# Kernel tuning notes

Hardware: AMD Instinct MI355X
Metric: run time of the kernel (lower is better)

## Reference

```python
import jax, jax.numpy as jnp
import numpy as np

BN_EPS = 1e-5


def _mlp_layer(x, W, b, gamma, beta):
    # x: [B, N, Cin]; Conv1d(k=1) == per-point linear, then BatchNorm1d over (B,N), ReLU
    y = jnp.einsum('bnc,oc->bno', x, W) + b  # [B, N, Cout]
    mean = y.mean(axis=(0, 1))
    var = y.var(axis=(0, 1))
    y = (y - mean) * jax.lax.rsqrt(var + BN_EPS) * gamma + beta
    return jax.nn.relu(y)


def setup_inputs() -> dict:
    key = jax.random.key(0)
    ks = jax.random.split(key, 12)
    B, N, M, C1, C2 = 4, 16384, 4096, 64, 256
    Cin = C1 + C2  # 320
    H1, H2 = 256, 128
    inp = {
        'xyz_fine': jax.random.normal(ks[0], (B, N, 3), jnp.float32),
        'xyz_coarse': jax.random.normal(ks[1], (B, M, 3), jnp.float32),
        'feats_fine': jax.random.normal(ks[2], (B, N, C1), jnp.float32),
        'feats_coarse': jax.random.normal(ks[3], (B, M, C2), jnp.float32),
        'W1': jax.random.normal(ks[4], (H1, Cin), jnp.float32) * (1.0 / np.sqrt(Cin)),
        'b1': jnp.zeros((H1,), jnp.float32),
        'g1': jnp.ones((H1,), jnp.float32),
        'be1': jnp.zeros((H1,), jnp.float32),
        'W2': jax.random.normal(ks[5], (H2, H1), jnp.float32) * (1.0 / np.sqrt(H1)),
        'b2': jnp.zeros((H2,), jnp.float32),
        'g2': jnp.ones((H2,), jnp.float32),
        'be2': jnp.zeros((H2,), jnp.float32),
    }
    return inp


def reference(xyz_fine, xyz_coarse, feats_fine, feats_coarse,
              W1, b1, g1, be1, W2, b2, g2, be2):
    # squared pairwise distance: [B, N, M]
    d = (jnp.sum(xyz_fine ** 2, -1, keepdims=True)
         - 2.0 * jnp.einsum('bnd,bmd->bnm', xyz_fine, xyz_coarse)
         + jnp.sum(xyz_coarse ** 2, -1)[:, None, :])
    # 3 smallest distances
    neg_d, idx = jax.lax.top_k(-d, 3)        # idx: [B, N, 3]
    dists = jnp.maximum(-neg_d, 1e-10)
    w = 1.0 / dists
    w = w / jnp.sum(w, -1, keepdims=True)    # [B, N, 3]
    # gather coarse features: [B, N, 3, C2]
    gathered = jax.vmap(lambda f, i: f[i])(feats_coarse, idx)
    interp = jnp.einsum('bnk,bnkc->bnc', w, gathered)  # [B, N, C2]
    x = jnp.concatenate([interp, feats_fine], axis=-1)  # [B, N, Cin]
    x = _mlp_layer(x, W1, b1, g1, be1)
    x = _mlp_layer(x, W2, b2, g2, be2)
    return x  # [B, N, 128]
```

## Files before the change

kernel.cpp:

```cpp
#include <hip/hip_runtime.h>
#include <hip/hip_bf16.h>
#include <stdint.h>

#define B_    4
#define N_    16384
#define M_    4096
#define C1_   64
#define C2_   256
#define CIN_  320
#define H1_   256
#define H2_   128
#define ROWS_ (B_*N_)
#define SPLIT_ 4
#define CHUNK_ (M_/SPLIT_)

typedef __attribute__((ext_vector_type(8))) short bf16x8;
typedef __attribute__((ext_vector_type(4))) float f32x4;
typedef __attribute__((ext_vector_type(8))) unsigned short u16x8;
typedef __attribute__((ext_vector_type(4))) unsigned short u16x4;

static __device__ __forceinline__ unsigned short f2bf(float f) {
  union { float f; unsigned u; } v; v.f = f;
  unsigned r = v.u + 0x7fffu + ((v.u >> 16) & 1u);
  return (unsigned short)(r >> 16);
}
static __device__ __forceinline__ float bf2f(unsigned short h) {
  union { unsigned u; float f; } v; v.u = ((unsigned)h) << 16;
  return v.f;
}

static __device__ __forceinline__ void gload16(const void* g, void* lds) {
  __builtin_amdgcn_global_load_lds(
      (__attribute__((address_space(1))) void*)(uintptr_t)g,
      (__attribute__((address_space(3))) void*)(uintptr_t)lds,
      16, 0, 0);
}

#define INS3(dv, iv) do {                                        \
  float _d = (dv); int _ii = (iv);                               \
  if (_d < d3) {                                                 \
    if (_d < d2) {                                               \
      d3 = d2; i3 = i2;                                          \
      if (_d < d1) { d2 = d1; i2 = i1; d1 = _d; i1 = _ii; }      \
      else         { d2 = _d; i2 = _ii; }                        \
    } else { d3 = _d; i3 = _ii; }                                \
  } } while (0)

__global__ __launch_bounds__(256) void prep(
    const float* __restrict__ W1, const float* __restrict__ W2,
    const float* __restrict__ xyzc, const float* __restrict__ fc,
    unsigned short* __restrict__ W1b, unsigned short* __restrict__ W2b,
    float4* __restrict__ cpk, unsigned short* __restrict__ fcb)
{
  int i = blockIdx.x * 256 + threadIdx.x;
  if (i < H1_*CIN_) W1b[i] = f2bf(W1[i]);
  if (i < H2_*H1_)  W2b[i] = f2bf(W2[i]);
  if (i < B_*M_) {
    float x = xyzc[i*3], y = xyzc[i*3+1], z = xyzc[i*3+2];
    cpk[i] = make_float4(x, y, z, x*x + y*y + z*z);
  }
  const int total4 = B_*M_*C2_/4;
  const int stride = gridDim.x * 256;
  for (int t = i; t < total4; t += stride) {
    float4 v = ((const float4*)fc)[t];
    u16x4 o;
    o[0] = f2bf(v.x); o[1] = f2bf(v.y); o[2] = f2bf(v.z); o[3] = f2bf(v.w);
    ((u16x4*)fcb)[t] = o;
  }
}

__global__ __launch_bounds__(256) void nn_scan(
    const float* __restrict__ xyzf, const float4* __restrict__ cpk,
    float4* __restrict__ pdw, int4* __restrict__ piw)
{
  __shared__ float4 cp[CHUNK_];
  const int tid  = threadIdx.x;
  const int s    = blockIdx.x & (SPLIT_-1);
  const int tile = (blockIdx.x >> 2) & 63;
  const int b    = blockIdx.x >> 8;

  const float4* src = cpk + (size_t)b * M_ + s * CHUNK_;
  for (int i = tid; i < CHUNK_; i += 256) cp[i] = src[i];
  __syncthreads();

  const int p = tile * 256 + tid;
  const size_t gp = (size_t)b * N_ + p;
  const float* xf = xyzf + gp * 3;
  const float fx = xf[0], fy = xf[1], fz = xf[2];
  const float xx = fx*fx + fy*fy + fz*fz;
  const float nx = -2.f*fx, ny = -2.f*fy, nz = -2.f*fz;

  float d1 = 3.4e38f, d2 = 3.4e38f, d3 = 3.4e38f;
  int   i1 = 0, i2 = 0, i3 = 0;

  #pragma unroll 1
  for (int g = 0; g < CHUNK_; g += 8) {
    float dd[8];
    #pragma unroll
    for (int u = 0; u < 8; ++u) {
      float4 c = cp[g + u];
      dd[u] = xx + fmaf(nx, c.x, fmaf(ny, c.y, fmaf(nz, c.z, c.w)));
    }
    #pragma unroll
    for (int u = 0; u < 8; ++u) {
      float d = dd[u]; int j = g + u;
      if (d < d3) {
        bool c1 = d < d1, c2 = d < d2;
        d3 = c2 ? d2 : d;              i3 = c2 ? i2 : j;
        d2 = c1 ? d1 : (c2 ? d : d2);  i2 = c1 ? i1 : (c2 ? j : i2);
        d1 = c1 ? d  : d1;             i1 = c1 ? j  : i1;
      }
    }
  }
  const int base = s * CHUNK_;
  pdw[(size_t)s * ROWS_ + gp] = make_float4(d1, d2, d3, 0.f);
  piw[(size_t)s * ROWS_ + gp] = make_int4(i1 + base, i2 + base, i3 + base, 0);
}

__global__ __launch_bounds__(256) void nn_finish(
    const float4* __restrict__ pdw, const int4* __restrict__ piw,
    const float* __restrict__ ff, const unsigned short* __restrict__ fcb,
    unsigned short* __restrict__ X)
{
  __shared__ float wv[64][3];
  __shared__ int   wi[64][3];
  const int tid  = threadIdx.x;
  const int b    = blockIdx.x >> 8;
  const int tile = blockIdx.x & 255;
  const size_t gp0 = (size_t)b * N_ + tile * 64;

  if (tid < 64) {
    const size_t gp = gp0 + tid;
    float d1 = 3.4e38f, d2 = 3.4e38f, d3 = 3.4e38f;
    int   i1 = 0, i2 = 0, i3 = 0;
    #pragma unroll
    for (int s = 0; s < SPLIT_; ++s) {
      float4 dv = pdw[(size_t)s * ROWS_ + gp];
      int4   iv = piw[(size_t)s * ROWS_ + gp];
      INS3(dv.x, iv.x);
      INS3(dv.y, iv.y);
      INS3(dv.z, iv.z);
    }
    d1 = fmaxf(d1, 1e-10f); d2 = fmaxf(d2, 1e-10f); d3 = fmaxf(d3, 1e-10f);
    float u1 = 1.f/d1, u2 = 1.f/d2, u3 = 1.f/d3;
    float inv = 1.f/(u1 + u2 + u3);
    wv[tid][0] = u1*inv; wv[tid][1] = u2*inv; wv[tid][2] = u3*inv;
    wi[tid][0] = i1;     wi[tid][1] = i2;     wi[tid][2] = i3;
  }
  __syncthreads();

  const int w = tid >> 6, l = tid & 63;
  const unsigned short* fcb_b = fcb + (size_t)b * M_ * C2_;
  unsigned short* Xb = X + gp0 * CIN_;
  #pragma unroll 2
  for (int q = 0; q < 16; ++q) {
    int pl = w * 16 + q;
    float a1 = wv[pl][0], a2 = wv[pl][1], a3 = wv[pl][2];
    int   j1 = wi[pl][0], j2 = wi[pl][1], j3 = wi[pl][2];
    u16x4 r1 = ((const u16x4*)(fcb_b + (size_t)j1 * C2_))[l];
    u16x4 r2 = ((const u16x4*)(fcb_b + (size_t)j2 * C2_))[l];
    u16x4 r3 = ((const u16x4*)(fcb_b + (size_t)j3 * C2_))[l];
    u16x4 o;
    #pragma unroll
    for (int e = 0; e < 4; ++e) {
      float v = fmaf(a1, bf2f(r1[e]), fmaf(a2, bf2f(r2[e]), a3 * bf2f(r3[e])));
      o[e] = f2bf(v);
    }
    *(u16x4*)(Xb + (size_t)pl * CIN_ + l * 4) = o;
  }

  {
    const float* ffb = ff + gp0 * C1_;
    int pl = tid >> 2, c0 = (tid & 3) * 16;
    const float4* fsrc = (const float4*)(ffb + (size_t)pl * C1_ + c0);
    unsigned short* dst = Xb + (size_t)pl * CIN_ + C2_ + c0;
    #pragma unroll
    for (int t = 0; t < 4; ++t) {
      float4 v = fsrc[t];
      u16x4 o;
      o[0] = f2bf(v.x); o[1] = f2bf(v.y); o[2] = f2bf(v.z); o[3] = f2bf(v.w);
      *(u16x4*)(dst + t * 4) = o;
    }
  }
}

template<int K, int NTOT, bool OUTBF>
__global__ __launch_bounds__(256) void gemm_stats(
    const unsigned short* __restrict__ A,
    const unsigned short* __restrict__ Bw,
    unsigned short* __restrict__ Yb,
    float* __restrict__ Yf,
    float* __restrict__ part)
{
  constexpr int BM = 128, BN = 128, BK = 64;
  constexpr int NCT = NTOT / BN;
  __shared__ unsigned short As[BM*BK];
  __shared__ unsigned short Bs[BN*BK];
  __shared__ float sred[2][BN][2];

  const int tid = threadIdx.x;
  const int l   = tid & 63;
  const int w   = tid >> 6;
  const int wm  = w >> 1, wn = w & 1;
  int rt, ct;
  if (NCT == 2) {
    rt = (blockIdx.x & 7) | ((blockIdx.x >> 4) << 3);
    ct = (blockIdx.x >> 3) & 1;
  } else {
    rt = blockIdx.x / NCT; ct = blockIdx.x % NCT;
  }
  const int lr  = l & 15;
  const int lk  = (l >> 4) * 8;

  const unsigned short* Arow = A  + (size_t)rt * BM * K;
  const unsigned short* Brow = Bw + (size_t)ct * BN * K;

  f32x4 acc[4][4] = {};

  for (int k0 = 0; k0 < K; k0 += BK) {
    #pragma unroll
    for (int q = 0; q < 4; ++q) {
      int chunk = q * 256 + tid;
      int row = chunk >> 3, cc = chunk & 7;
      unsigned ldsoff = (unsigned)(q * 256 + (tid & ~63)) * 16u;
      gload16(Arow + (size_t)row * K + k0 + cc * 8, (char*)As + ldsoff);
      gload16(Brow + (size_t)row * K + k0 + cc * 8, (char*)Bs + ldsoff);
    }
    __syncthreads();
    #pragma unroll
    for (int kk = 0; kk < BK/32; ++kk) {
      bf16x8 af[4], bfr[4];
      #pragma unroll
      for (int m = 0; m < 4; ++m)
        af[m] = *(const bf16x8*)(As + (wm*64 + m*16 + lr)*BK + kk*32 + lk);
      #pragma unroll
      for (int n = 0; n < 4; ++n)
        bfr[n] = *(const bf16x8*)(Bs + (wn*64 + n*16 + lr)*BK + kk*32 + lk);
      #pragma unroll
      for (int m = 0; m < 4; ++m)
        #pragma unroll
        for (int n = 0; n < 4; ++n)
          acc[m][n] = __builtin_amdgcn_mfma_f32_16x16x32_bf16(af[m], bfr[n], acc[m][n], 0, 0, 0);
    }
    __syncthreads();
  }

  const int orow0 = rt*BM + wm*64;
  const int ocol0 = ct*BN + wn*64;
  #pragma unroll
  for (int n = 0; n < 4; ++n) {
    float s = 0.f, qq = 0.f;
    #pragma unroll
    for (int m = 0; m < 4; ++m) {
      #pragma unroll
      for (int r = 0; r < 4; ++r) {
        float v = acc[m][n][r];
        int row = orow0 + m*16 + (l >> 4)*4 + r;
        int col = ocol0 + n*16 + lr;
        size_t off = (size_t)row * NTOT + col;
        if (OUTBF) Yb[off] = f2bf(v); else Yf[off] = v;
        s += v; qq += v*v;
      }
    }
    s  += __shfl_xor(s, 16);  s  += __shfl_xor(s, 32);
    qq += __shfl_xor(qq, 16); qq += __shfl_xor(qq, 32);
    if (l < 16) {
      sred[wm][wn*64 + n*16 + l][0] = s;
      sred[wm][wn*64 + n*16 + l][1] = qq;
    }
  }
  __syncthreads();
  if (tid < BN) {
    float S = sred[0][tid][0] + sred[1][tid][0];
    float Q = sred[0][tid][1] + sred[1][tid][1];
    part[((size_t)rt * NTOT + ct*BN + tid) * 2 + 0] = S;
    part[((size_t)rt * NTOT + ct*BN + tid) * 2 + 1] = Q;
  }
}

template<int K, int NTOT>
__global__ __launch_bounds__(256) void gemm_bnrelu_stats(
    const unsigned short* __restrict__ Yin,
    const float* __restrict__ ab,
    const unsigned short* __restrict__ Bw,
    unsigned short* __restrict__ Yb,
    float* __restrict__ part)
{
  constexpr int BM = 128, BN = 128, BK = 64;
  constexpr int NCT = NTOT / BN;
  __shared__ unsigned short As[BM*BK];
  __shared__ unsigned short Bs[BN*BK];
  __shared__ float sa[K], sb[K];
  __shared__ float sred[2][BN][2];

  const int tid = threadIdx.x;
  const int l   = tid & 63;
  const int w   = tid >> 6;
  const int wm  = w >> 1, wn = w & 1;
  const int rt  = blockIdx.x / NCT, ct = blockIdx.x % NCT;
  const int lr  = l & 15;
  const int lk  = (l >> 4) * 8;
  const int cc  = tid & 7;
  const int r0  = tid >> 3;

  sa[tid] = ab[tid*2];
  sb[tid] = ab[tid*2 + 1];

  const unsigned short* Arow = Yin + (size_t)rt * BM * K;
  const unsigned short* Brow = Bw  + (size_t)ct * BN * K;

  f32x4 acc[4][4] = {};
  __syncthreads();

  for (int k0 = 0; k0 < K; k0 += BK) {
    #pragma unroll
    for (int q = 0; q < 4; ++q) {
      int chunk = q * 256 + tid;
      int row = chunk >> 3, c8 = chunk & 7;
      unsigned ldsoff = (unsigned)(q * 256 + (tid & ~63)) * 16u;
      gload16(Brow + (size_t)row * K + k0 + c8 * 8, (char*)Bs + ldsoff);
    }
    float a_[8], b_[8];
    *(float4*)&a_[0] = *(const float4*)&sa[k0 + cc*8];
    *(float4*)&a_[4] = *(const float4*)&sa[k0 + cc*8 + 4];
    *(float4*)&b_[0] = *(const float4*)&sb[k0 + cc*8];
    *(float4*)&b_[4] = *(const float4*)&sb[k0 + cc*8 + 4];
    #pragma unroll
    for (int q = 0; q < 4; ++q) {
      int row = q*32 + r0;
      u16x8 v = *(const u16x8*)(Arow + (size_t)row * K + k0 + cc*8);
      u16x8 o;
      #pragma unroll
      for (int e = 0; e < 8; ++e) {
        float f = fmaxf(fmaf(bf2f((unsigned short)v[e]), a_[e], b_[e]), 0.f);
        o[e] = f2bf(f);
      }
      *(u16x8*)((char*)As + (unsigned)(q*256 + tid) * 16u) = o;
    }
    __syncthreads();
    #pragma unroll
    for (int kk = 0; kk < BK/32; ++kk) {
      bf16x8 af[4], bfr[4];
      #pragma unroll
      for (int m = 0; m < 4; ++m)
        af[m] = *(const bf16x8*)(As + (wm*64 + m*16 + lr)*BK + kk*32 + lk);
      #pragma unroll
      for (int n = 0; n < 4; ++n)
        bfr[n] = *(const bf16x8*)(Bs + (wn*64 + n*16 + lr)*BK + kk*32 + lk);
      #pragma unroll
      for (int m = 0; m < 4; ++m)
        #pragma unroll
        for (int n = 0; n < 4; ++n)
          acc[m][n] = __builtin_amdgcn_mfma_f32_16x16x32_bf16(af[m], bfr[n], acc[m][n], 0, 0, 0);
    }
    __syncthreads();
  }

  const int orow0 = rt*BM + wm*64;
  const int ocol0 = ct*BN + wn*64;
  #pragma unroll
  for (int n = 0; n < 4; ++n) {
    float s = 0.f, qq = 0.f;
    #pragma unroll
    for (int m = 0; m < 4; ++m) {
      #pragma unroll
      for (int r = 0; r < 4; ++r) {
        float v = acc[m][n][r];
        int row = orow0 + m*16 + (l >> 4)*4 + r;
        int col = ocol0 + n*16 + lr;
        Yb[(size_t)row * NTOT + col] = f2bf(v);
        s += v; qq += v*v;
      }
    }
    s  += __shfl_xor(s, 16);  s  += __shfl_xor(s, 32);
    qq += __shfl_xor(qq, 16); qq += __shfl_xor(qq, 32);
    if (l < 16) {
      sred[wm][wn*64 + n*16 + l][0] = s;
      sred[wm][wn*64 + n*16 + l][1] = qq;
    }
  }
  __syncthreads();
  if (tid < BN) {
    float S = sred[0][tid][0] + sred[1][tid][0];
    float Q = sred[0][tid][1] + sred[1][tid][1];
    part[((size_t)rt * NTOT + ct*BN + tid) * 2 + 0] = S;
    part[((size_t)rt * NTOT + ct*BN + tid) * 2 + 1] = Q;
  }
}

__global__ void finalize_stats(const float* __restrict__ part,
                               const float* __restrict__ g,
                               const float* __restrict__ be,
                               float* __restrict__ ab, int nrt, int C, float invM)
{
  const int c = blockIdx.x;
  const int t = threadIdx.x;
  float s = 0.f, q = 0.f;
  for (int r = t; r < nrt; r += 64) {
    s += part[((size_t)r * C + c) * 2 + 0];
    q += part[((size_t)r * C + c) * 2 + 1];
  }
  #pragma unroll
  for (int o = 32; o > 0; o >>= 1) { s += __shfl_down(s, o); q += __shfl_down(q, o); }
  if (t == 0) {
    float mean = s * invM;
    float var  = q * invM - mean * mean;
    float rstd = rsqrtf(var + 1e-5f);
    float a = g[c] * rstd;
    ab[c*2 + 0] = a;
    ab[c*2 + 1] = be[c] - mean * a;
  }
}

__global__ __launch_bounds__(256) void bnrelu_out(
    const unsigned short* __restrict__ Y, const float* __restrict__ ab,
    float* __restrict__ out)
{
  __shared__ float sa[H2_], sb[H2_];
  if (threadIdx.x < H2_) { sa[threadIdx.x] = ab[threadIdx.x*2]; sb[threadIdx.x] = ab[threadIdx.x*2+1]; }
  __syncthreads();
  const size_t total = (size_t)ROWS_ * H2_ / 8;
  for (size_t i = (size_t)blockIdx.x*256 + threadIdx.x; i < total; i += (size_t)gridDim.x*256) {
    u16x8 v = ((const u16x8*)Y)[i];
    int cb = (int)((i * 8) & (H2_ - 1));
    float4 o0, o1;
    o0.x = fmaxf(fmaf(bf2f((unsigned short)v[0]), sa[cb+0], sb[cb+0]), 0.f);
    o0.y = fmaxf(fmaf(bf2f((unsigned short)v[1]), sa[cb+1], sb[cb+1]), 0.f);
    o0.z = fmaxf(fmaf(bf2f((unsigned short)v[2]), sa[cb+2], sb[cb+2]), 0.f);
    o0.w = fmaxf(fmaf(bf2f((unsigned short)v[3]), sa[cb+3], sb[cb+3]), 0.f);
    o1.x = fmaxf(fmaf(bf2f((unsigned short)v[4]), sa[cb+4], sb[cb+4]), 0.f);
    o1.y = fmaxf(fmaf(bf2f((unsigned short)v[5]), sa[cb+5], sb[cb+5]), 0.f);
    o1.z = fmaxf(fmaf(bf2f((unsigned short)v[6]), sa[cb+6], sb[cb+6]), 0.f);
    o1.w = fmaxf(fmaf(bf2f((unsigned short)v[7]), sa[cb+7], sb[cb+7]), 0.f);
    ((float4*)out)[i*2]   = o0;
    ((float4*)out)[i*2+1] = o1;
  }
}

extern "C" void kernel_launch(void* const* d_in, const int* in_sizes, int n_in,
                              void* d_out, int out_size, void* d_ws, size_t ws_size,
                              hipStream_t stream)
{
  const float* xyzf = (const float*)d_in[0];
  const float* xyzc = (const float*)d_in[1];
  const float* ff   = (const float*)d_in[2];
  const float* fc   = (const float*)d_in[3];
  const float* W1   = (const float*)d_in[4];
  const float* g1   = (const float*)d_in[6];
  const float* be1  = (const float*)d_in[7];
  const float* W2   = (const float*)d_in[8];
  const float* g2   = (const float*)d_in[10];
  const float* be2  = (const float*)d_in[11];
  float* out = (float*)d_out;

  char* ws = (char*)d_ws;
  unsigned short* W1b  = (unsigned short*)(ws + 0);
  unsigned short* W2b  = (unsigned short*)(ws + 163840);
  unsigned short* X    = (unsigned short*)(ws + 229376);
  unsigned short* Y2b  = (unsigned short*)(ws + 229376);
  unsigned short* fcb  = (unsigned short*)(ws + 42172416);
  unsigned short* Y1   = (unsigned short*)(ws + 42172416);
  float* part1 = (float*)(ws + 75726848);
  float* part2 = (float*)(ws + 76775424);
  float* ab1   = (float*)(ws + 77299712);
  float* ab2   = (float*)(ws + 77301760);
  float4* cpk  = (float4*)(ws + 77302784);
  float4* pdw  = (float4*)(ws + 77564928);
  int4*   piw  = (int4*)  (ws + 85953536);

  prep<<<1024, 256, 0, stream>>>(W1, W2, xyzc, fc, W1b, W2b, cpk, fcb);
  nn_scan<<<B_ * 64 * SPLIT_, 256, 0, stream>>>(xyzf, cpk, pdw, piw);
  nn_finish<<<B_ * 256, 256, 0, stream>>>(pdw, piw, ff, fcb, X);

  gemm_stats<CIN_, H1_, true><<<(ROWS_/128) * (H1_/128), 256, 0, stream>>>(
      X, W1b, Y1, nullptr, part1);
  finalize_stats<<<H1_, 64, 0, stream>>>(part1, g1, be1, ab1, ROWS_/128, H1_, 1.f/ROWS_);

  gemm_bnrelu_stats<H1_, H2_><<<(ROWS_/128) * (H2_/128), 256, 0, stream>>>(
      Y1, ab1, W2b, Y2b, part2);
  finalize_stats<<<H2_, 64, 0, stream>>>(part2, g2, be2, ab2, ROWS_/128, H2_, 1.f/ROWS_);
  bnrelu_out<<<2048, 256, 0, stream>>>(Y2b, ab2, out);
}
```

Baseline: 163.2 us.

## Replace brute-force 3-NN scan with x-sorted sweep and pruned bidirectional search

Adds a per-batch bitonic sort of coarse points by x coordinate. The brute-force distance scan is replaced by a binary search into the sorted list, followed by two directional sweeps, one per block parity, that stop once the x-gap squared exceeds the current third-best distance. This avoids most of the O(N*M) distance evaluations. In exchange it adds a single-block-per-batch sort kernel and divergent, data-dependent loop lengths. Distances are now computed directly rather than via the expanded form, which can change tie behaviour slightly.

```diff
diff --git a/kernel.cpp b/kernel.cpp
--- a/kernel.cpp
+++ b/kernel.cpp
@@ -11,8 +11,7 @@
 #define H1_   256
 #define H2_   128
 #define ROWS_ (B_*N_)
-#define SPLIT_ 4
-#define CHUNK_ (M_/SPLIT_)
+#define SPLIT_ 2
 
 typedef __attribute__((ext_vector_type(8))) short bf16x8;
 typedef __attribute__((ext_vector_type(4))) float f32x4;
@@ -69,52 +68,109 @@
   }
 }
 
-__global__ __launch_bounds__(256) void nn_scan(
-    const float* __restrict__ xyzf, const float4* __restrict__ cpk,
+__global__ __launch_bounds__(1024) void sort_coarse(
+    const float4* __restrict__ cpk,
+    float* __restrict__ sxs, float4* __restrict__ cps)
+{
+  __shared__ unsigned long long key[M_];
+  const int b = blockIdx.x;
+  const int tid = threadIdx.x;
+  for (int i = tid; i < M_; i += 1024) {
+    unsigned ux = __float_as_uint(cpk[(size_t)b*M_ + i].x);
+    ux ^= (ux >> 31) ? 0xFFFFFFFFu : 0x80000000u;
+    key[i] = ((unsigned long long)ux << 32) | (unsigned)i;
+  }
+  __syncthreads();
+  for (int k = 2; k <= M_; k <<= 1) {
+    for (int j = k >> 1; j > 0; j >>= 1) {
+      for (int i = tid; i < M_; i += 1024) {
+        int ixj = i ^ j;
+        if (ixj > i) {
+          unsigned long long a = key[i], c = key[ixj];
+          bool up = ((i & k) == 0);
+          if ((a > c) == up) { key[i] = c; key[ixj] = a; }
+        }
+      }
+      __syncthreads();
+    }
+  }
+  for (int i = tid; i < M_; i += 1024) {
+    int idx = (int)(unsigned)key[i];
+    float4 c = cpk[(size_t)b*M_ + idx];
+    sxs[(size_t)b*M_ + i] = c.x;
+    cps[(size_t)b*M_ + i] = make_float4(c.x, c.y, c.z, __int_as_float(idx));
+  }
+}
+
+__global__ __launch_bounds__(256) void nn_scan_sorted(
+    const float* __restrict__ xyzf, const float* __restrict__ sxs,
+    const float4* __restrict__ cps,
     float4* __restrict__ pdw, int4* __restrict__ piw)
 {
-  __shared__ float4 cp[CHUNK_];
+  __shared__ float sx_l[M_];
   const int tid  = threadIdx.x;
-  const int s    = blockIdx.x & (SPLIT_-1);
-  const int tile = (blockIdx.x >> 2) & 63;
-  const int b    = blockIdx.x >> 8;
-
-  const float4* src = cpk + (size_t)b * M_ + s * CHUNK_;
-  for (int i = tid; i < CHUNK_; i += 256) cp[i] = src[i];
+  const int dir  = blockIdx.x & 1;
+  const int tile = (blockIdx.x >> 1) & 63;
+  const int b    = blockIdx.x >> 7;
+
+  const float4* srcx = (const float4*)(sxs + (size_t)b * M_);
+  for (int i = tid; i < M_/4; i += 256) ((float4*)sx_l)[i] = srcx[i];
   __syncthreads();
 
   const int p = tile * 256 + tid;
   const size_t gp = (size_t)b * N_ + p;
   const float* xf = xyzf + gp * 3;
-  const float fx = xf[0], fy = xf[1], fz = xf[2];
-  const float xx = fx*fx + fy*fy + fz*fz;
-  const float nx = -2.f*fx, ny = -2.f*fy, nz = -2.f*fz;
-
-  float d1 = 3.4e38f, d2 = 3.4e38f, d3 = 3.4e38f;
-  int   i1 = 0, i2 = 0, i3 = 0;
-
-  #pragma unroll 1
-  for (int g = 0; g < CHUNK_; g += 8) {
-    float dd[8];
-    #pragma unroll
-    for (int u = 0; u < 8; ++u) {
-      float4 c = cp[g + u];
-      dd[u] = xx + fmaf(nx, c.x, fmaf(ny, c.y, fmaf(nz, c.z, c.w)));
-    }
-    #pragma unroll
-    for (int u = 0; u < 8; ++u) {
-      float d = dd[u]; int j = g + u;
-      if (d < d3) {
-        bool c1 = d < d1, c2 = d < d2;
-        d3 = c2 ? d2 : d;              i3 = c2 ? i2 : j;
-        d2 = c1 ? d1 : (c2 ? d : d2);  i2 = c1 ? i1 : (c2 ? j : i2);
-        d1 = c1 ? d  : d1;             i1 = c1 ? j  : i1;
+  const float px = xf[0], py = xf[1], pz = xf[2];
+
+  int lo = 0, hi = M_;
+  while (lo < hi) { int mid = (lo + hi) >> 1; if (sx_l[mid] < px) lo = mid + 1; else hi = mid; }
+
+  float D1 = 3.4e38f, D2 = 3.4e38f, D3 = 3.4e38f;
+  int   I1 = 0, I2 = 0, I3 = 0;
+  const float4* cpsb = cps + (size_t)b * M_;
+
+#define TRY_INSERT(cvec, okflag) do {                                     \
+    float ax = (cvec).x - px, ay = (cvec).y - py, az = (cvec).z - pz;     \
+    float d = fmaf(ax, ax, fmaf(ay, ay, az * az));                        \
+    int idx = __float_as_int((cvec).w);                                   \
+    if ((okflag) && d < D3) {                                             \
+      bool c1 = d < D1, c2 = d < D2;                                      \
+      D3 = c2 ? D2 : d;             I3 = c2 ? I2 : idx;                   \
+      D2 = c1 ? D1 : (c2 ? d : D2); I2 = c1 ? I1 : (c2 ? idx : I2);       \
+      D1 = c1 ? d  : D1;            I1 = c1 ? idx : I1;                   \
+    } } while (0)
+
+  if (dir == 0) {
+    #pragma unroll 1
+    for (int j0 = lo; j0 < M_; j0 += 4) {
+      float dx0 = sx_l[j0] - px;
+      if (dx0 * dx0 >= D3) break;
+      #pragma unroll
+      for (int e = 0; e < 4; ++e) {
+        int j = j0 + e;
+        bool ok = j < M_;
+        float4 c = cpsb[ok ? j : M_ - 1];
+        TRY_INSERT(c, ok);
       }
     }
-  }
-  const int base = s * CHUNK_;
-  pdw[(size_t)s * ROWS_ + gp] = make_float4(d1, d2, d3, 0.f);
-  piw[(size_t)s * ROWS_ + gp] = make_int4(i1 + base, i2 + base, i3 + base, 0);
+  } else {
+    #pragma unroll 1
+    for (int j0 = lo - 1; j0 >= 0; j0 -= 4) {
+      float dx0 = px - sx_l[j0];
+      if (dx0 * dx0 >= D3) break;
+      #pragma unroll
+      for (int e = 0; e < 4; ++e) {
+        int j = j0 - e;
+        bool ok = j >= 0;
+        float4 c = cpsb[ok ? j : 0];
+        TRY_INSERT(c, ok);
+      }
+    }
+  }
+#undef TRY_INSERT
+
+  pdw[(size_t)dir * ROWS_ + gp] = make_float4(D1, D2, D3, 0.f);
+  piw[(size_t)dir * ROWS_ + gp] = make_int4(I1, I2, I3, 0);
 }
 
 __global__ __launch_bounds__(256) void nn_finish(
@@ -467,9 +523,12 @@
   float4* cpk  = (float4*)(ws + 77302784);
   float4* pdw  = (float4*)(ws + 77564928);
   int4*   piw  = (int4*)  (ws + 85953536);
+  float4* cps  = (float4*)(ws + 88051712);
+  float*  sxs  = (float*) (ws + 88313856);
 
   prep<<<1024, 256, 0, stream>>>(W1, W2, xyzc, fc, W1b, W2b, cpk, fcb);
-  nn_scan<<<B_ * 64 * SPLIT_, 256, 0, stream>>>(xyzf, cpk, pdw, piw);
+  sort_coarse<<<B_, 1024, 0, stream>>>(cpk, sxs, cps);
+  nn_scan_sorted<<<B_ * 64 * 2, 256, 0, stream>>>(xyzf, sxs, cps, pdw, piw);
   nn_finish<<<B_ * 256, 256, 0, stream>>>(pdw, piw, ff, fcb, X);
 
   gemm_stats<CIN_, H1_, true><<<(ROWS_/128) * (H1_/128), 256, 0, stream>>>(
```

New measurement: 588.4 us (median of 2 runs). 3.6x slower.
